# Kernel optimization log

Measured on AMD Instinct MI355X. Metric: run time of the kernel, lower is better.

## Reference

```python
import jax, jax.numpy as jnp
import numpy as np

T, N, D, L, H = 128, 256, 256, 3, 4


def _ln(x, s, b):
    m = jnp.mean(x, axis=-1, keepdims=True)
    v = jnp.mean((x - m) ** 2, axis=-1, keepdims=True)
    return (x - m) / jnp.sqrt(v + 1e-5) * s + b


def setup_inputs() -> dict:
    key = jax.random.key(0)
    ks = jax.random.split(key, 12)
    s = 0.05
    d = D
    return {
        "spatial_states": jax.random.normal(ks[0], (T, N, d), jnp.float32),
        "re_norm": jax.random.uniform(ks[1], (), jnp.float32),
        "sensor_time": jnp.cumsum(jax.random.uniform(ks[2], (T,), jnp.float32) * 0.1),
        "re_proj_w": jax.random.normal(ks[3], (d, 1), jnp.float32) * s,
        "re_proj_b": jnp.zeros((d,), jnp.float32),
        "tb_n1_s": jnp.ones((d,), jnp.float32),
        "tb_n1_b": jnp.zeros((d,), jnp.float32),
        "tb_in_w": jax.random.normal(ks[4], (3 * d, d), jnp.float32) * s,
        "tb_in_b": jnp.zeros((3 * d,), jnp.float32),
        "tb_out_w": jax.random.normal(ks[5], (d, d), jnp.float32) * s,
        "tb_out_b": jnp.zeros((d,), jnp.float32),
        "tb_n2_s": jnp.ones((d,), jnp.float32),
        "tb_n2_b": jnp.zeros((d,), jnp.float32),
        "tb_ff1_w": jax.random.normal(ks[6], (2 * d, d), jnp.float32) * s,
        "tb_ff1_b": jnp.zeros((2 * d,), jnp.float32),
        "tb_ff2_w": jax.random.normal(ks[7], (d, 2 * d), jnp.float32) * s,
        "tb_ff2_b": jnp.zeros((d,), jnp.float32),
        "cell_ff1_w": jax.random.normal(ks[8], (L, d, 2 * d), jnp.float32) * s,
        "cell_ff1_b": jnp.zeros((L, d), jnp.float32),
        "cell_ff2_w": jax.random.normal(ks[9], (L, d, 2 * d), jnp.float32) * s,
        "cell_ff2_b": jnp.zeros((L, d), jnp.float32),
        "cell_logtau": jnp.tile(jnp.linspace(-1.0, 1.0, d, dtype=jnp.float32), (L, 1)),
        "cell_tb_w": jax.random.normal(ks[10], (L, d, 2 * d), jnp.float32) * s,
        "cell_tb_b": jnp.zeros((L, d), jnp.float32),
    }


def reference(spatial_states, re_norm, sensor_time,
              re_proj_w, re_proj_b,
              tb_n1_s, tb_n1_b, tb_in_w, tb_in_b, tb_out_w, tb_out_b,
              tb_n2_s, tb_n2_b, tb_ff1_w, tb_ff1_b, tb_ff2_w, tb_ff2_b,
              cell_ff1_w, cell_ff1_b, cell_ff2_w, cell_ff2_b,
              cell_logtau, cell_tb_w, cell_tb_b):
    t, n, d = spatial_states.shape
    nL = cell_logtau.shape[0]
    hd = d // H

    # dt per step: first absolute time, then diffs (as in torch source)
    dts = jnp.concatenate([sensor_time[:1], sensor_time[1:] - sensor_time[:-1]])  # [T]
    re_bias = re_proj_w[:, 0] * re_norm + re_proj_b  # [d]

    def token_block(x):  # x: [T, N, d]; attention over N, batched over T
        y = _ln(x, tb_n1_s, tb_n1_b)
        qkv = y @ tb_in_w.T + tb_in_b
        q, k, v = jnp.split(qkv, 3, axis=-1)
        q = q.reshape(t, n, H, hd)
        k = k.reshape(t, n, H, hd)
        v = v.reshape(t, n, H, hd)
        logits = jnp.einsum('bqhd,bkhd->bhqk', q, k) / jnp.sqrt(jnp.float32(hd))
        a = jax.nn.softmax(logits, axis=-1)
        o = jnp.einsum('bhqk,bkhd->bqhd', a, v).reshape(t, n, d)
        x = x + (o @ tb_out_w.T + tb_out_b)
        y = _ln(x, tb_n2_s, tb_n2_b)
        f = jax.nn.silu(y @ tb_ff1_w.T + tb_ff1_b) @ tb_ff2_w.T + tb_ff2_b
        return x + f

    seq = spatial_states
    for l in range(nL):
        # token attention + re_bias are independent of the recurrence -> vectorize over T
        xs = token_block(seq) + re_bias  # [T, N, d]
        w1, b1 = cell_ff1_w[l], cell_ff1_b[l]
        w2, b2 = cell_ff2_w[l], cell_ff2_b[l]
        wt, bt = cell_tb_w[l], cell_tb_b[l]
        tau = jnp.exp(cell_logtau[l])  # [d]

        def step(h, xd):
            x_t, dt = xd
            xh = jnp.concatenate([x_t, h], axis=-1)  # [N, 2d]
            f1 = jnp.tanh(xh @ w1.T + b1)
            f2 = jnp.tanh(xh @ w2.T + b2)
            gate = jax.nn.sigmoid(-tau * dt + (xh @ wt.T + bt))
            h_new = gate * f1 + (1.0 - gate) * f2
            return h_new, h_new

        h0 = jnp.zeros((n, d), seq.dtype)
        _, outs = jax.lax.scan(step, h0, (xs, dts))  # outs: [T, N, d]
        seq = outs + seq if l > 0 else outs
    return seq
```

## Files before the change

### kernel.cpp

```cpp
#include <hip/hip_runtime.h>


#define T_DIM 128
#define N_DIM 256
#define D_DIM 256
#define H_DIM 4
#define HD_DIM 64
#define L_DIM 3
#define TN (T_DIM * N_DIM)
#define SCAN_SEQ 2

typedef __bf16 bf16x8 __attribute__((ext_vector_type(8)));
typedef __bf16 bf16x4 __attribute__((ext_vector_type(4)));
typedef float f32x4 __attribute__((ext_vector_type(4)));

#define LDS_BAR()                                            \
  do {                                                       \
    asm volatile("s_waitcnt lgkmcnt(0)" ::: "memory");       \
    __builtin_amdgcn_s_barrier();                            \
    __builtin_amdgcn_sched_barrier(0);                       \
  } while (0)

__device__ inline float wave_reduce_sum(float v) {
#pragma unroll
  for (int off = 32; off > 0; off >>= 1) v += __shfl_xor(v, off);
  return v;
}

__device__ inline float bf_to_f(unsigned short u) {
  return __uint_as_float((unsigned int)u << 16);
}

__global__ __launch_bounds__(256) void ln_kernel(const float* __restrict__ x,
                                                 const float* __restrict__ sc,
                                                 const float* __restrict__ bi,
                                                 __bf16* __restrict__ y) {
  const int wid = threadIdx.x >> 6;
  const int lane = threadIdx.x & 63;
  const size_t row = (size_t)blockIdx.x * 4 + wid;
  const float4 xv = *(const float4*)(x + row * D_DIM + lane * 4);
  float s = xv.x + xv.y + xv.z + xv.w;
  float ss = xv.x * xv.x + xv.y * xv.y + xv.z * xv.z + xv.w * xv.w;
  s = wave_reduce_sum(s);
  ss = wave_reduce_sum(ss);
  const float mean = s * (1.f / D_DIM);
  const float var = ss * (1.f / D_DIM) - mean * mean;
  const float r = rsqrtf(var + 1e-5f);
  const float4 scv = *(const float4*)(sc + lane * 4);
  const float4 biv = *(const float4*)(bi + lane * 4);
  bf16x4 ov;
  ov[0] = (__bf16)((xv.x - mean) * r * scv.x + biv.x);
  ov[1] = (__bf16)((xv.y - mean) * r * scv.y + biv.y);
  ov[2] = (__bf16)((xv.z - mean) * r * scv.z + biv.z);
  ov[3] = (__bf16)((xv.w - mean) * r * scv.w + biv.w);
  *(bf16x4*)(y + row * D_DIM + lane * 4) = ov;
}

template <int EPI, int OBF>
__global__ __launch_bounds__(256) void gemm_tiled(const __bf16* __restrict__ A,
                                                  const __bf16* __restrict__ W,
                                                  const float* __restrict__ bias,
                                                  const float* __restrict__ R,
                                                  void* __restrict__ outv,
                                                  int M, int Nout, int K) {
  __shared__ __bf16 a_lds[128][72];
  __shared__ __bf16 b_lds[128][72];
  const int tid = threadIdx.x;
  const int w = tid >> 6, l = tid & 63;
  const int lr = l & 15, kg = l >> 4;
  const int wm = (w & 1) * 64, wn = (w >> 1) * 64;
  const int m0 = blockIdx.x * 128, n0 = blockIdx.y * 128;
  const int srow = tid >> 1, scol = (tid & 1) * 32;
  const __bf16* ag = A + (size_t)(m0 + srow) * K + scol;
  const __bf16* bg = W + (size_t)(n0 + srow) * K + scol;

  bf16x8 av[4], bv[4];
#pragma unroll
  for (int c = 0; c < 4; ++c) {
    av[c] = *(const bf16x8*)(ag + c * 8);
    bv[c] = *(const bf16x8*)(bg + c * 8);
  }

  f32x4 acc[4][4] = {};
  for (int k0 = 0; k0 < K; k0 += 64) {
    LDS_BAR();
#pragma unroll
    for (int c = 0; c < 4; ++c) {
      *(bf16x8*)&a_lds[srow][scol + c * 8] = av[c];
      *(bf16x8*)&b_lds[srow][scol + c * 8] = bv[c];
    }
    if (k0 + 64 < K) {
#pragma unroll
      for (int c = 0; c < 4; ++c) {
        av[c] = *(const bf16x8*)(ag + k0 + 64 + c * 8);
        bv[c] = *(const bf16x8*)(bg + k0 + 64 + c * 8);
      }
    }
    LDS_BAR();
#pragma unroll
    for (int ks = 0; ks < 2; ++ks) {
      bf16x8 af[4], bf[4];
#pragma unroll
      for (int mt = 0; mt < 4; ++mt)
        af[mt] = *(const bf16x8*)&a_lds[wm + mt * 16 + lr][ks * 32 + kg * 8];
#pragma unroll
      for (int nt = 0; nt < 4; ++nt)
        bf[nt] = *(const bf16x8*)&b_lds[wn + nt * 16 + lr][ks * 32 + kg * 8];
#pragma unroll
      for (int mt = 0; mt < 4; ++mt)
#pragma unroll
        for (int nt = 0; nt < 4; ++nt)
          acc[mt][nt] =
              __builtin_amdgcn_mfma_f32_16x16x32_bf16(af[mt], bf[nt], acc[mt][nt], 0, 0, 0);
    }
  }
#pragma unroll
  for (int nt = 0; nt < 4; ++nt) {
    const int col = n0 + wn + nt * 16 + lr;
    const float bvs = bias[col];
#pragma unroll
    for (int mt = 0; mt < 4; ++mt) {
#pragma unroll
      for (int j = 0; j < 4; ++j) {
        const int row = m0 + wm + mt * 16 + kg * 4 + j;
        float v = acc[mt][nt][j] + bvs;
        if (EPI == 1) v += R[(size_t)row * Nout + col];
        if (EPI == 2) v = v * (1.f / (1.f + __expf(-v)));
        const size_t oi = (size_t)row * Nout + col;
        if (OBF)
          ((__bf16*)outv)[oi] = (__bf16)v;
        else
          ((float*)outv)[oi] = v;
      }
    }
  }
}

__global__ __launch_bounds__(256, 2) void attn_mfma(const __bf16* __restrict__ qkv,
                                                    __bf16* __restrict__ o) {
  const int t = blockIdx.x, h = blockIdx.y;
  const int tid = threadIdx.x;
  const int w = tid >> 6, l = tid & 63;
  const int lr = l & 15, kg = l >> 4;

  __shared__ __bf16 vt_lds[64 * 256];
  __shared__ __bf16 p_lds[4][16 * 256];

  {
    const __bf16* vrow = qkv + ((size_t)(t * N_DIM + tid)) * 768 + 512 + h * HD_DIM;
#pragma unroll
    for (int c8 = 0; c8 < 64; c8 += 8) {
      bf16x8 v = *(const bf16x8*)(vrow + c8);
#pragma unroll
      for (int i = 0; i < 8; ++i) {
        const int c = c8 + i;
        const int byte = (c * 512 + tid * 2) ^ ((c & 7) << 4);
        *(__bf16*)((char*)vt_lds + byte) = v[i];
      }
    }
  }
  __syncthreads();

  const __bf16* kbase = qkv + (size_t)t * N_DIM * 768 + 256 + h * HD_DIM;
  const __bf16* qbase = qkv + (size_t)t * N_DIM * 768 + h * HD_DIM;
  char* pw = (char*)&p_lds[w][0];

  for (int qt = 0; qt < 4; ++qt) {
    const int q0 = w * 64 + qt * 16;
    const bf16x8 qf0 = *(const bf16x8*)(qbase + (size_t)(q0 + lr) * 768 + kg * 8);
    const bf16x8 qf1 = *(const bf16x8*)(qbase + (size_t)(q0 + lr) * 768 + 32 + kg * 8);
    f32x4 acc[16];
#pragma unroll
    for (int nt = 0; nt < 16; ++nt) {
      const bf16x8 a0 = *(const bf16x8*)(kbase + (size_t)(nt * 16 + lr) * 768 + kg * 8);
      const bf16x8 a1 = *(const bf16x8*)(kbase + (size_t)(nt * 16 + lr) * 768 + 32 + kg * 8);
      f32x4 s = {};
      s = __builtin_amdgcn_mfma_f32_16x16x32_bf16(a0, qf0, s, 0, 0, 0);
      s = __builtin_amdgcn_mfma_f32_16x16x32_bf16(a1, qf1, s, 0, 0, 0);
      acc[nt] = s;
    }
    float mx = -3.0e38f;
#pragma unroll
    for (int nt = 0; nt < 16; ++nt)
#pragma unroll
      for (int j = 0; j < 4; ++j) mx = fmaxf(mx, acc[nt][j]);
    mx = fmaxf(mx, __shfl_xor(mx, 16));
    mx = fmaxf(mx, __shfl_xor(mx, 32));
    float sum = 0.f;
#pragma unroll
    for (int nt = 0; nt < 16; ++nt) {
      bf16x4 pb;
#pragma unroll
      for (int j = 0; j < 4; ++j) {
        const float p = __expf((acc[nt][j] - mx) * 0.125f);
        pb[j] = (__bf16)p;
        sum += (float)pb[j];
      }
      const int byte = (lr * 512 + nt * 32 + kg * 8) ^ ((lr & 7) << 4);
      *(bf16x4*)(pw + byte) = pb;
    }
    sum += __shfl_xor(sum, 16);
    sum += __shfl_xor(sum, 32);
    const float inv = 1.f / sum;
    f32x4 oacc[4] = {};
#pragma unroll
    for (int kt = 0; kt < 8; ++kt) {
      const int pbyte = (lr * 512 + kt * 64 + kg * 16) ^ ((lr & 7) << 4);
      const bf16x8 bfrag = *(const bf16x8*)(pw + pbyte);
#pragma unroll
      for (int ct = 0; ct < 4; ++ct) {
        const int c = ct * 16 + lr;
        const int vbyte = (c * 512 + kt * 64 + kg * 16) ^ ((c & 7) << 4);
        const bf16x8 afrag = *(const bf16x8*)((char*)vt_lds + vbyte);
        oacc[ct] = __builtin_amdgcn_mfma_f32_16x16x32_bf16(afrag, bfrag, oacc[ct], 0, 0, 0);
      }
    }
    __bf16* orow = o + ((size_t)(t * N_DIM + q0 + lr)) * D_DIM + h * HD_DIM;
#pragma unroll
    for (int ct = 0; ct < 4; ++ct) {
      bf16x4 ov;
#pragma unroll
      for (int j = 0; j < 4; ++j) ov[j] = (__bf16)(oacc[ct][j] * inv);
      *(bf16x4*)(orow + ct * 16 + kg * 4) = ov;
    }
  }
}

__global__ __launch_bounds__(512) void scan_mfma(const __bf16* __restrict__ P,
                                                 const __bf16* __restrict__ Wh,
                                                 const float* __restrict__ logtau,
                                                 const float* __restrict__ st,
                                                 const float* __restrict__ addsrc,
                                                 float* __restrict__ out) {
  const int tid = threadIdx.x;
  const int w = tid >> 6, l = tid & 63;
  const int lr = l & 15, kg = l >> 4;
  const int n0 = blockIdx.x * SCAN_SEQ;

  __shared__ float acc_lds[SCAN_SEQ][772];
  __shared__ __bf16 h_lds[2][264];
  __shared__ float dts[T_DIM];

  if (tid < T_DIM) dts[tid] = (tid == 0) ? st[0] : st[tid] - st[tid - 1];
  if (tid < 66) ((bf16x8*)h_lds)[tid] = (bf16x8){};

  bf16x8 wreg[6][8];
  {
    const __bf16* wb = Wh + (size_t)(w * 96 + lr) * 256 + kg * 8;
#pragma unroll
    for (int nt = 0; nt < 6; ++nt)
#pragma unroll
      for (int kt = 0; kt < 8; ++kt)
        wreg[nt][kt] = *(const bf16x8*)(wb + (size_t)nt * 16 * 256 + kt * 32);
  }
  __syncthreads();

  const int s = tid >> 8;
  const int d = tid & 255;
  const float tau = __expf(logtau[d]);
  const unsigned short* Pp = (const unsigned short*)P + (size_t)(n0 + s) * 768 + d;
  float* op = out + (size_t)(n0 + s) * D_DIM + d;
  const float* ap = addsrc ? addsrc + (size_t)(n0 + s) * D_DIM + d : nullptr;
  const char* hbase = (const char*)&h_lds[0][0] + (lr & 1) * 528 + kg * 16;

  unsigned short c1 = Pp[0], c2 = Pp[256], c3 = Pp[512];
  unsigned short n1 = 0, n2 = 0, n3 = 0;
  {
    const unsigned short* Pn = Pp + (size_t)N_DIM * 768;
    n1 = Pn[0]; n2 = Pn[256]; n3 = Pn[512];
  }
  float av = ap ? ap[0] : 0.f;
  float nav = ap ? ap[(size_t)N_DIM * D_DIM] : 0.f;

  for (int t = 0; t < T_DIM; ++t) {
    unsigned short m1 = 0, m2 = 0, m3 = 0;
    float mav = 0.f;
    if (t + 2 < T_DIM) {
      const unsigned short* Pm = Pp + (size_t)(t + 2) * N_DIM * 768;
      m1 = Pm[0]; m2 = Pm[256]; m3 = Pm[512];
      if (ap) mav = ap[(size_t)(t + 2) * N_DIM * D_DIM];
    }

    f32x4 acc[6] = {};
#pragma unroll
    for (int kt = 0; kt < 8; ++kt) {
      const bf16x8 a = *(const bf16x8*)(hbase + kt * 64);
#pragma unroll
      for (int nt = 0; nt < 6; ++nt)
        acc[nt] = __builtin_amdgcn_mfma_f32_16x16x32_bf16(a, wreg[nt][kt], acc[nt], 0, 0, 0);
    }
    if (l < 16) {
#pragma unroll
      for (int nt = 0; nt < 6; ++nt)
#pragma unroll
      for (int j = 0; j < SCAN_SEQ; ++j)
        acc_lds[j][w * 96 + nt * 16 + lr] = acc[nt][j];
    }
    LDS_BAR();

    const float dt = dts[t];
    const float a1 = acc_lds[s][d] + bf_to_f(c1);
    const float a2 = acc_lds[s][256 + d] + bf_to_f(c2);
    const float a3 = acc_lds[s][512 + d] + bf_to_f(c3) - tau * dt;
    const float e1 = __expf(-2.f * fabsf(a1));
    const float f1 = copysignf((1.f - e1) / (1.f + e1), a1);
    const float e2 = __expf(-2.f * fabsf(a2));
    const float f2 = copysignf((1.f - e2) / (1.f + e2), a2);
    const float g = 1.f / (1.f + __expf(-a3));
    const float hn = g * f1 + (1.f - g) * f2;
    h_lds[s][d] = (__bf16)hn;
    op[(size_t)t * N_DIM * D_DIM] = hn + av;
    LDS_BAR();

    c1 = n1; c2 = n2; c3 = n3; av = nav;
    n1 = m1; n2 = m2; n3 = m3; nav = mav;
  }
}

__global__ void cvt_kernel(const float* __restrict__ src, __bf16* __restrict__ dst, int n) {
  const int i = blockIdx.x * 256 + threadIdx.x;
  if (i < n) dst[i] = (__bf16)src[i];
}

__global__ void pack_cell_kernel(const float* __restrict__ w1, const float* __restrict__ w2,
                                 const float* __restrict__ wt, __bf16* __restrict__ Wx,
                                 __bf16* __restrict__ Whb) {
  const int idx = blockIdx.x * 256 + threadIdx.x;
  if (idx >= 3 * 768 * 256) return;
  const int l = idx / (768 * 256);
  const int r2 = idx - l * (768 * 256);
  const int jj = r2 >> 8;
  const int c = r2 & 255;
  const int m = jj >> 8;
  const int r = jj & 255;
  const float* src = (m == 0 ? w1 : (m == 1 ? w2 : wt)) + ((size_t)l * 256 + r) * 512;
  Wx[(size_t)l * (768 * 256) + (size_t)jj * 256 + c] = (__bf16)src[c];
  Whb[(size_t)l * (768 * 256) + (size_t)jj * 256 + c] = (__bf16)src[256 + c];
}

__global__ void bias_pack_kernel(const float* __restrict__ b1, const float* __restrict__ b2,
                                 const float* __restrict__ bt, const float* __restrict__ ff2b,
                                 const float* __restrict__ rw, const float* __restrict__ rb,
                                 const float* __restrict__ rn, float* __restrict__ bias768,
                                 float* __restrict__ ff2bias) {
  const int idx = blockIdx.x * 256 + threadIdx.x;
  if (idx < 3 * 768) {
    const int l = idx / 768, jj = idx % 768, m = jj >> 8, r = jj & 255;
    const float* s = (m == 0 ? b1 : (m == 1 ? b2 : bt));
    bias768[idx] = s[l * 256 + r];
  }
  if (idx < 256) ff2bias[idx] = ff2b[idx] + rw[idx] * rn[0] + rb[idx];
}

extern "C" void kernel_launch(void* const* d_in, const int* in_sizes, int n_in,
                              void* d_out, int out_size, void* d_ws, size_t ws_size,
                              hipStream_t stream) {
  (void)in_sizes; (void)n_in; (void)out_size; (void)ws_size;
  const float* spatial = (const float*)d_in[0];
  const float* re_norm = (const float*)d_in[1];
  const float* sensor_time = (const float*)d_in[2];
  const float* re_proj_w = (const float*)d_in[3];
  const float* re_proj_b = (const float*)d_in[4];
  const float* n1s = (const float*)d_in[5];
  const float* n1b = (const float*)d_in[6];
  const float* in_w = (const float*)d_in[7];
  const float* in_b = (const float*)d_in[8];
  const float* out_w = (const float*)d_in[9];
  const float* out_b = (const float*)d_in[10];
  const float* n2s = (const float*)d_in[11];
  const float* n2b = (const float*)d_in[12];
  const float* ff1_w = (const float*)d_in[13];
  const float* ff1_b = (const float*)d_in[14];
  const float* ff2_w = (const float*)d_in[15];
  const float* ff2_b = (const float*)d_in[16];
  const float* c1w = (const float*)d_in[17];
  const float* c1b = (const float*)d_in[18];
  const float* c2w = (const float*)d_in[19];
  const float* c2b = (const float*)d_in[20];
  const float* clt = (const float*)d_in[21];
  const float* ctw = (const float*)d_in[22];
  const float* ctb = (const float*)d_in[23];

  char* ws = (char*)d_ws;
  size_t off = 0;
  auto alloc = [&](size_t b) {
    char* p = ws + off;
    off = (off + b + 255) & ~(size_t)255;
    return p;
  };
  float* seq = (float*)alloc((size_t)TN * D_DIM * 4);
  float* xb = (float*)alloc((size_t)TN * D_DIM * 4);
  __bf16* yb = (__bf16*)alloc((size_t)TN * D_DIM * 2);
  char* big = (char*)alloc((size_t)TN * 768 * 2);
  __bf16* qkvb = (__bf16*)big;
  __bf16* gb = (__bf16*)big;
  __bf16* Pb = (__bf16*)big;
  __bf16* w_in = (__bf16*)alloc(768 * 256 * 2);
  __bf16* w_out = (__bf16*)alloc(256 * 256 * 2);
  __bf16* w_f1 = (__bf16*)alloc(512 * 256 * 2);
  __bf16* w_f2 = (__bf16*)alloc(256 * 512 * 2);
  __bf16* Wx = (__bf16*)alloc((size_t)3 * 768 * 256 * 2);
  __bf16* Whb = (__bf16*)alloc((size_t)3 * 768 * 256 * 2);
  float* b768 = (float*)alloc(3 * 768 * 4);
  float* f2bias = (float*)alloc(256 * 4);

  cvt_kernel<<<(768 * 256 + 255) / 256, 256, 0, stream>>>(in_w, w_in, 768 * 256);
  cvt_kernel<<<(256 * 256 + 255) / 256, 256, 0, stream>>>(out_w, w_out, 256 * 256);
  cvt_kernel<<<(512 * 256 + 255) / 256, 256, 0, stream>>>(ff1_w, w_f1, 512 * 256);
  cvt_kernel<<<(256 * 512 + 255) / 256, 256, 0, stream>>>(ff2_w, w_f2, 256 * 512);
  pack_cell_kernel<<<(3 * 768 * 256 + 255) / 256, 256, 0, stream>>>(c1w, c2w, ctw, Wx, Whb);
  bias_pack_kernel<<<9, 256, 0, stream>>>(c1b, c2b, ctb, ff2_b, re_proj_w, re_proj_b,
                                          re_norm, b768, f2bias);

  for (int l = 0; l < L_DIM; ++l) {
    const float* seq_in = (l == 0) ? spatial : seq;
    ln_kernel<<<TN / 4, 256, 0, stream>>>(seq_in, n1s, n1b, yb);
    gemm_tiled<0, 1><<<dim3(TN / 128, 768 / 128), 256, 0, stream>>>(yb, w_in, in_b, nullptr,
                                                                    qkvb, TN, 768, 256);
    attn_mfma<<<dim3(T_DIM, H_DIM), 256, 0, stream>>>(qkvb, yb);
    gemm_tiled<1, 0><<<dim3(TN / 128, 256 / 128), 256, 0, stream>>>(yb, w_out, out_b, seq_in,
                                                                    xb, TN, 256, 256);
    ln_kernel<<<TN / 4, 256, 0, stream>>>(xb, n2s, n2b, yb);
    gemm_tiled<2, 1><<<dim3(TN / 128, 512 / 128), 256, 0, stream>>>(yb, w_f1, ff1_b, nullptr,
                                                                    gb, TN, 512, 256);
    gemm_tiled<1, 1><<<dim3(TN / 128, 256 / 128), 256, 0, stream>>>(gb, w_f2, f2bias, xb, yb,
                                                                    TN, 256, 512);
    gemm_tiled<0, 1><<<dim3(TN / 128, 768 / 128), 256, 0, stream>>>(
        yb, Wx + (size_t)l * 768 * 256, b768 + l * 768, nullptr, Pb, TN, 768, 256);
    float* outp = (l == 2) ? (float*)d_out : seq;
    const float* addp = (l == 0) ? nullptr : seq;
    scan_mfma<<<N_DIM / SCAN_SEQ, 512, 0, stream>>>(Pb, Whb + (size_t)l * 768 * 256,
                                                    clt + l * 256, sensor_time, addp, outp);
  }
}
```

Baseline: 1.203 ms.

## Process one sequence per scan block with four waves holding full weight slice

The recurrent scan kernel now handles one sequence per block with 256 threads, instead of two sequences per block with 512 threads. This launches twice as many blocks, so more compute units can work on the scan. The cost is that each wave now holds twice as many recurrent weight fragments in registers (12x8 bf16x8). Each wave also issues twice as many MFMAs per time step, which lengthens the serial per-step latency and raises register pressure or spill risk.

```diff
diff --git a/kernel.cpp b/kernel.cpp
--- a/kernel.cpp
+++ b/kernel.cpp
@@ -8,7 +8,6 @@
 #define HD_DIM 64
 #define L_DIM 3
 #define TN (T_DIM * N_DIM)
-#define SCAN_SEQ 2
 
 typedef __bf16 bf16x8 __attribute__((ext_vector_type(8)));
 typedef __bf16 bf16x4 __attribute__((ext_vector_type(4)));
@@ -226,42 +225,41 @@
   }
 }
 
-__global__ __launch_bounds__(512) void scan_mfma(const __bf16* __restrict__ P,
-                                                 const __bf16* __restrict__ Wh,
-                                                 const float* __restrict__ logtau,
-                                                 const float* __restrict__ st,
-                                                 const float* __restrict__ addsrc,
-                                                 float* __restrict__ out) {
+__global__ __launch_bounds__(256, 1) void scan_mfma(const __bf16* __restrict__ P,
+                                                    const __bf16* __restrict__ Wh,
+                                                    const float* __restrict__ logtau,
+                                                    const float* __restrict__ st,
+                                                    const float* __restrict__ addsrc,
+                                                    float* __restrict__ out) {
   const int tid = threadIdx.x;
   const int w = tid >> 6, l = tid & 63;
   const int lr = l & 15, kg = l >> 4;
-  const int n0 = blockIdx.x * SCAN_SEQ;
-
-  __shared__ float acc_lds[SCAN_SEQ][772];
-  __shared__ __bf16 h_lds[2][264];
+  const int n = blockIdx.x;
+
+  __shared__ float acc2[776];
+  __shared__ __bf16 h_lds[264];
   __shared__ float dts[T_DIM];
 
   if (tid < T_DIM) dts[tid] = (tid == 0) ? st[0] : st[tid] - st[tid - 1];
-  if (tid < 66) ((bf16x8*)h_lds)[tid] = (bf16x8){};
-
-  bf16x8 wreg[6][8];
+  if (tid < 33) ((bf16x8*)h_lds)[tid] = (bf16x8){};
+
+  bf16x8 wreg[12][8];
   {
-    const __bf16* wb = Wh + (size_t)(w * 96 + lr) * 256 + kg * 8;
-#pragma unroll
-    for (int nt = 0; nt < 6; ++nt)
+    const __bf16* wb = Wh + (size_t)(w * 192 + lr) * 256 + kg * 8;
+#pragma unroll
+    for (int nt = 0; nt < 12; ++nt)
 #pragma unroll
       for (int kt = 0; kt < 8; ++kt)
         wreg[nt][kt] = *(const bf16x8*)(wb + (size_t)nt * 16 * 256 + kt * 32);
   }
   __syncthreads();
 
-  const int s = tid >> 8;
-  const int d = tid & 255;
+  const int d = tid;
   const float tau = __expf(logtau[d]);
-  const unsigned short* Pp = (const unsigned short*)P + (size_t)(n0 + s) * 768 + d;
-  float* op = out + (size_t)(n0 + s) * D_DIM + d;
-  const float* ap = addsrc ? addsrc + (size_t)(n0 + s) * D_DIM + d : nullptr;
-  const char* hbase = (const char*)&h_lds[0][0] + (lr & 1) * 528 + kg * 16;
+  const unsigned short* Pp = (const unsigned short*)P + (size_t)n * 768 + d;
+  float* op = out + (size_t)n * D_DIM + d;
+  const float* ap = addsrc ? addsrc + (size_t)n * D_DIM + d : nullptr;
+  const char* hbase = (const char*)h_lds + kg * 16;
 
   unsigned short c1 = Pp[0], c2 = Pp[256], c3 = Pp[512];
   unsigned short n1 = 0, n2 = 0, n3 = 0;
@@ -281,34 +279,31 @@
       if (ap) mav = ap[(size_t)(t + 2) * N_DIM * D_DIM];
     }
 
-    f32x4 acc[6] = {};
+    f32x4 acc[12] = {};
 #pragma unroll
     for (int kt = 0; kt < 8; ++kt) {
       const bf16x8 a = *(const bf16x8*)(hbase + kt * 64);
 #pragma unroll
-      for (int nt = 0; nt < 6; ++nt)
+      for (int nt = 0; nt < 12; ++nt)
         acc[nt] = __builtin_amdgcn_mfma_f32_16x16x32_bf16(a, wreg[nt][kt], acc[nt], 0, 0, 0);
     }
     if (l < 16) {
 #pragma unroll
-      for (int nt = 0; nt < 6; ++nt)
-#pragma unroll
-      for (int j = 0; j < SCAN_SEQ; ++j)
-        acc_lds[j][w * 96 + nt * 16 + lr] = acc[nt][j];
+      for (int nt = 0; nt < 12; ++nt) acc2[w * 192 + nt * 16 + lr] = acc[nt][0];
     }
     LDS_BAR();
 
     const float dt = dts[t];
-    const float a1 = acc_lds[s][d] + bf_to_f(c1);
-    const float a2 = acc_lds[s][256 + d] + bf_to_f(c2);
-    const float a3 = acc_lds[s][512 + d] + bf_to_f(c3) - tau * dt;
+    const float a1 = acc2[d] + bf_to_f(c1);
+    const float a2 = acc2[256 + d] + bf_to_f(c2);
+    const float a3 = acc2[512 + d] + bf_to_f(c3) - tau * dt;
     const float e1 = __expf(-2.f * fabsf(a1));
     const float f1 = copysignf((1.f - e1) / (1.f + e1), a1);
     const float e2 = __expf(-2.f * fabsf(a2));
     const float f2 = copysignf((1.f - e2) / (1.f + e2), a2);
     const float g = 1.f / (1.f + __expf(-a3));
     const float hn = g * f1 + (1.f - g) * f2;
-    h_lds[s][d] = (__bf16)hn;
+    h_lds[d] = (__bf16)hn;
     op[(size_t)t * N_DIM * D_DIM] = hn + av;
     LDS_BAR();
 
@@ -429,7 +424,7 @@
         yb, Wx + (size_t)l * 768 * 256, b768 + l * 768, nullptr, Pb, TN, 768, 256);
     float* outp = (l == 2) ? (float*)d_out : seq;
     const float* addp = (l == 0) ? nullptr : seq;
-    scan_mfma<<<N_DIM / SCAN_SEQ, 512, 0, stream>>>(Pb, Whb + (size_t)l * 768 * 256,
-                                                    clt + l * 256, sensor_time, addp, outp);
-  }
-}
+    scan_mfma<<<N_DIM, 256, 0, stream>>>(Pb, Whb + (size_t)l * 768 * 256,
+                                         clt + l * 256, sensor_time, addp, outp);
+  }
+}
```

After: 1.337 ms. +11.1%, slower.
